# Kernel optimization log

Hardware: AMD Instinct MI355X
Metric: run time of the kernel (lower is better)

The kernel has to match this reference:

```python
import jax, jax.numpy as jnp
import numpy as np
import math

D_MODEL = 1024
NUM_HEADS = 16
D_HEAD = D_MODEL // NUM_HEADS


def setup_inputs() -> dict:
    key = jax.random.key(0)
    ks = jax.random.split(key, 15)
    B, S, D = 2, 2048, D_MODEL
    s = 1.0 / math.sqrt(D)
    inp = {
        'query': jax.random.normal(ks[0], (B, S, D), jnp.float32),
        'key': jax.random.normal(ks[1], (B, S, D), jnp.float32),
        'value': jax.random.normal(ks[2], (B, S, D), jnp.float32),
        'pos_embedding': jax.random.normal(ks[3], (B, S, D), jnp.float32),
        'Wq': jax.random.normal(ks[4], (D, D), jnp.float32) * s,
        'bq': jnp.zeros((D,), jnp.float32),
        'Wk': jax.random.normal(ks[5], (D, D), jnp.float32) * s,
        'bk': jnp.zeros((D,), jnp.float32),
        'Wv': jax.random.normal(ks[6], (D, D), jnp.float32) * s,
        'bv': jnp.zeros((D,), jnp.float32),
        'Wp': jax.random.normal(ks[7], (D, D), jnp.float32) * s,
        'bp': jnp.zeros((D,), jnp.float32),
        'Wo': jax.random.normal(ks[8], (D, D), jnp.float32) * s,
        'bo': jnp.zeros((D,), jnp.float32),
    }
    return inp


def _relative_shift(pos_score):
    # pos_score: [B, H, S1, S2] -> Transformer-XL pad/reshape/slice shift
    B, H, S1, S2 = pos_score.shape
    padded = jnp.pad(pos_score, ((0, 0), (0, 0), (0, 0), (1, 0)))  # [B,H,S1,S2+1]
    padded = padded.reshape(B, H, S2 + 1, S1)
    return padded[:, :, 1:].reshape(B, H, S1, S2)


def reference(query, key, value, pos_embedding, Wq, bq, Wk, bk, Wv, bv, Wp, bp, Wo, bo):
    B, S, D = query.shape
    H, Dh = NUM_HEADS, D_HEAD
    sqrt_dim = math.sqrt(D)

    q = (query @ Wq.T + bq).reshape(B, S, H, Dh)          # [B,S,H,Dh]
    k = (key @ Wk.T + bk).reshape(B, S, H, Dh)            # [B,S,H,Dh]
    v = (value @ Wv.T + bv).reshape(B, S, H, Dh)          # [B,S,H,Dh]
    p = (pos_embedding @ Wp.T + bp).reshape(B, S, H, Dh)  # [B,S,H,Dh]

    content_score = jnp.einsum('bqhd,bkhd->bhqk', q, k)   # [B,H,S,S]
    pos_score = jnp.einsum('bqhd,bkhd->bhqk', q, p)       # [B,H,S,S]
    pos_score = _relative_shift(pos_score)

    score = (content_score + pos_score) / sqrt_dim
    attn = jax.nn.softmax(score, axis=-1)
    context = jnp.einsum('bhqk,bkhd->bqhd', attn, v).reshape(B, S, D)
    return context @ Wo.T + bo
```

## Files before the change

### kernel.cpp

```cpp
#include <hip/hip_runtime.h>
#include <hip/hip_bf16.h>

#define S_LEN  2048
#define DMODEL 1024
#define NHEADS 16
#define DHEAD  64
#define TOKENS 4096
#define QSCALE 0.04508422f

typedef __attribute__((ext_vector_type(8))) short bf16x8;
typedef __attribute__((ext_vector_type(4))) float f32x4;

template <int M> struct IC { static constexpr int value = M; };

__device__ __forceinline__ float bf2f(unsigned short b) {
    union { unsigned u; float f; } v; v.u = ((unsigned)b) << 16;
    return v.f;
}
__device__ __forceinline__ unsigned cvt_pk_bf16(float lo, float hi) {
    unsigned r;
    asm("v_cvt_pk_bf16_f32 %0, %1, %2" : "=v"(r) : "v"(lo), "v"(hi));
    return r;
}
__device__ __forceinline__ unsigned short f2bf1(float x) {
    return (unsigned short)cvt_pk_bf16(x, x);
}
__device__ __forceinline__ void lds_fence() {
    asm volatile("s_waitcnt lgkmcnt(0)" ::: "memory");
    __builtin_amdgcn_sched_barrier(0);
}
__device__ __forceinline__ void gload_lds16(const void* g, void* l) {
    __builtin_amdgcn_global_load_lds(
        (const __attribute__((address_space(1))) void*)g,
        (__attribute__((address_space(3))) void*)l, 16, 0, 0);
}

__global__ __launch_bounds__(256) void proj_gemm(
    const float* __restrict__ x0, const float* __restrict__ x1,
    const float* __restrict__ x2, const float* __restrict__ x3,
    const float* __restrict__ w0, const float* __restrict__ w1,
    const float* __restrict__ w2, const float* __restrict__ w3,
    const float* __restrict__ b0, const float* __restrict__ b1,
    const float* __restrict__ b2, const float* __restrict__ b3,
    unsigned short* __restrict__ o0, unsigned short* __restrict__ o1,
    unsigned short* __restrict__ o2, unsigned short* __restrict__ o3)
{
    const int z = blockIdx.z;
    const float* X  = (z == 0) ? x0 : (z == 1) ? x1 : (z == 2) ? x2 : x3;
    const float* W  = (z == 0) ? w0 : (z == 1) ? w1 : (z == 2) ? w2 : w3;
    const float* Bv = (z == 0) ? b0 : (z == 1) ? b1 : (z == 2) ? b2 : b3;
    unsigned short* O = (z == 0) ? o0 : (z == 1) ? o1 : (z == 2) ? o2 : o3;

    __shared__ __align__(16) unsigned short At[128 * 40];
    __shared__ __align__(16) unsigned short Bt[128 * 40];

    const int tid  = threadIdx.x;
    const int lane = tid & 63;
    const int w    = tid >> 6;
    const int wr   = w & 1, wc = w >> 1;
    const int m0   = blockIdx.x * 128;
    const int n0   = blockIdx.y * 128;
    const int l16  = lane & 15, lq = lane >> 4;

    f32x4 acc[4][4];
    #pragma unroll
    for (int i = 0; i < 4; i++)
        #pragma unroll
        for (int j = 0; j < 4; j++) acc[i][j] = (f32x4){0.f, 0.f, 0.f, 0.f};

    for (int k0 = 0; k0 < DMODEL; k0 += 32) {
        __syncthreads();
        #pragma unroll
        for (int i = 0; i < 4; i++) {
            int e = tid + i * 256;
            int row = e >> 3, cg = e & 7;
            float4 va = *(const float4*)&X[(long)(m0 + row) * DMODEL + k0 + cg * 4];
            uint2 ua; ua.x = cvt_pk_bf16(va.x, va.y); ua.y = cvt_pk_bf16(va.z, va.w);
            *(uint2*)&At[row * 40 + cg * 4] = ua;
            float4 vb = *(const float4*)&W[(long)(n0 + row) * DMODEL + k0 + cg * 4];
            uint2 ub; ub.x = cvt_pk_bf16(vb.x, vb.y); ub.y = cvt_pk_bf16(vb.z, vb.w);
            *(uint2*)&Bt[row * 40 + cg * 4] = ub;
        }
        __syncthreads();
        bf16x8 af[4], bfr[4];
        #pragma unroll
        for (int f = 0; f < 4; f++) {
            af[f]  = *(const bf16x8*)&At[(64 * wr + 16 * f + l16) * 40 + 8 * lq];
            bfr[f] = *(const bf16x8*)&Bt[(64 * wc + 16 * f + l16) * 40 + 8 * lq];
        }
        #pragma unroll
        for (int i = 0; i < 4; i++)
            #pragma unroll
            for (int j = 0; j < 4; j++)
                acc[i][j] = __builtin_amdgcn_mfma_f32_16x16x32_bf16(af[i], bfr[j], acc[i][j], 0, 0, 0);
    }

    #pragma unroll
    for (int j = 0; j < 4; j++) {
        int n_g = n0 + 64 * wc + 16 * j + l16;
        float bias = Bv[n_g];
        int h = n_g >> 6, dh = n_g & 63;
        if (z == 2) {
            #pragma unroll
            for (int i = 0; i < 4; i++) {
                int m_g = m0 + 64 * wr + 16 * i + 4 * lq;
                int b = m_g >> 11, s = m_g & (S_LEN - 1);
                uint2 u;
                u.x = cvt_pk_bf16(acc[i][j][0] + bias, acc[i][j][1] + bias);
                u.y = cvt_pk_bf16(acc[i][j][2] + bias, acc[i][j][3] + bias);
                *(uint2*)&O[(long)(((b * NHEADS + h) * DHEAD) + dh) * S_LEN + s] = u;
            }
        } else {
            float scale = (z == 0) ? QSCALE : 1.0f;
            #pragma unroll
            for (int i = 0; i < 4; i++) {
                #pragma unroll
                for (int r = 0; r < 4; r++) {
                    int m_g = m0 + 64 * wr + 16 * i + 4 * lq + r;
                    int b = m_g >> 11, s = m_g & (S_LEN - 1);
                    O[(long)(((b * NHEADS + h) * S_LEN) + s) * DHEAD + dh] =
                        f2bf1((acc[i][j][r] + bias) * scale);
                }
            }
        }
    }
}

__global__ __launch_bounds__(512, 4) void rel_attn(
    const unsigned short* __restrict__ Q,
    const unsigned short* __restrict__ K,
    const unsigned short* __restrict__ VT,
    const unsigned short* __restrict__ P,
    unsigned short* __restrict__ CTX)
{
    __shared__ __align__(16) unsigned short Kb[64 * 64];
    __shared__ __align__(16) unsigned short P2b[256 * 64];
    __shared__ __align__(16) unsigned short WPb[8 * 1344];

    const int tid  = threadIdx.x;
    const int lane = tid & 63;
    const int w    = tid >> 6;
    const int l16  = lane & 15;
    const int lq   = lane >> 4;

    const int wg = ((blockIdx.x & 7) << 6) | (blockIdx.x >> 3);
    const int qt = wg & 15;
    const int bh = wg >> 4;
    const int q0 = qt << 7;
    const long baseQK = (long)bh * (S_LEN * DHEAD);
    const int gq_rel = 16 * w + l16;

    const unsigned short* Kbh = K + baseQK;
    const unsigned short* Pbh = P + baseQK;
    const unsigned short* Vl  = VT + baseQK + (long)l16 * S_LEN + 8 * lq;

    const int gx0 = ((0 + lq) ^ (l16 & 7)) * 8;
    const int gx1 = ((4 + lq) ^ (l16 & 7)) * 8;

    bf16x8 qf0[2], qf1[2];
    {
        const unsigned short* qrow = Q + baseQK + (long)(q0 + gq_rel) * DHEAD + 8 * lq;
        qf0[0] = *(const bf16x8*)(qrow);
        qf0[1] = *(const bf16x8*)(qrow + 32);
        qf1[0] = *(const bf16x8*)(qrow + DHEAD);
        qf1[1] = *(const bf16x8*)(qrow + DHEAD + 32);
    }

    const int srow = lane >> 3;
    const int sgr  = (lane & 7) ^ srow;
    auto stage_K = [&](int kr0) __attribute__((always_inline)) {
        const unsigned short* src = Kbh + (long)(kr0 + w * 8 + srow) * 64 + sgr * 8;
        gload_lds16(src, &Kb[(w * 8) * 64]);
    };
    auto stage_P2 = [&](int mfirst) __attribute__((always_inline)) {
        int m = mfirst + w * 8 + srow;
        int pr = m - ((m >= 2049) ? 2049 : 0);
        const unsigned short* src = Pbh + (long)pr * 64 + sgr * 8;
        gload_lds16(src, &P2b[(((mfirst & 255)) + w * 8) * 64]);
    };

    float mrow = -1e30f, lrow = 0.f;
    f32x4 oacc[4];
    #pragma unroll
    for (int f = 0; f < 4; f++) oacc[f] = (f32x4){0.f, 0.f, 0.f, 0.f};

    unsigned short* tw        = &WPb[w * 1344 + l16 * 84 + 4 * lq];
    const unsigned short* tr  = &WPb[w * 1344 + l16 * 83 + 15 + 4 * lq];
    unsigned short* pw        = &WPb[w * 1344 + l16 * 72 + 4 * lq];
    const unsigned short* prd = &WPb[w * 1344 + l16 * 72 + 8 * lq];

    const int W0 = 1920 - q0;
    stage_K(0);
    stage_P2(W0); stage_P2(W0 + 64); stage_P2(W0 + 128);
    __syncthreads();

    auto finish = [&](float (&sc)[4][4], bf16x8 (&vf)[2][4]) __attribute__((always_inline)) {
        float tmax = sc[0][0];
        #pragma unroll
        for (int fc = 0; fc < 4; ++fc)
            #pragma unroll
            for (int r = 0; r < 4; ++r) tmax = fmaxf(tmax, sc[fc][r]);
        tmax = fmaxf(tmax, __shfl_xor(tmax, 16, 64));
        tmax = fmaxf(tmax, __shfl_xor(tmax, 32, 64));
        float nm = fmaxf(mrow, tmax);
        float alpha = __builtin_amdgcn_exp2f(mrow - nm);
        mrow = nm;
        float pv[4][4];
        float rs = 0.f;
        #pragma unroll
        for (int fc = 0; fc < 4; ++fc)
            #pragma unroll
            for (int r = 0; r < 4; ++r) {
                float p = __builtin_amdgcn_exp2f(sc[fc][r] - nm);
                pv[fc][r] = p;
                rs += p;
            }
        rs += __shfl_xor(rs, 16, 64);
        rs += __shfl_xor(rs, 32, 64);
        lrow = lrow * alpha + rs;
        #pragma unroll
        for (int f = 0; f < 4; f++)
            #pragma unroll
            for (int r = 0; r < 4; r++) oacc[f][r] *= alpha;

        lds_fence();
        #pragma unroll
        for (int fc = 0; fc < 4; ++fc) {
            uint2 u;
            u.x = cvt_pk_bf16(pv[fc][0], pv[fc][1]);
            u.y = cvt_pk_bf16(pv[fc][2], pv[fc][3]);
            *(uint2*)(pw + 16 * fc) = u;
        }
        lds_fence();
        bf16x8 pfr[2];
        pfr[0] = *(const bf16x8*)(prd);
        pfr[1] = *(const bf16x8*)(prd + 32);

        #pragma unroll
        for (int kk = 0; kk < 2; ++kk)
            #pragma unroll
            for (int fa = 0; fa < 4; ++fa)
                oacc[fa] = __builtin_amdgcn_mfma_f32_16x16x32_bf16(vf[kk][fa], pfr[kk], oacc[fa], 0, 0, 0);
    };

    auto tile_pure = [&](auto mc, int ct, bool dz) __attribute__((always_inline)) {
        constexpr int MODE = decltype(mc)::value;
        const int c0 = ct << 6;
        const int mb = c0 - q0 + 2032 - 16 * w + l16;

        f32x4 cacc[4];
        #pragma unroll
        for (int f = 0; f < 4; f++) cacc[f] = (f32x4){0.f, 0.f, 0.f, 0.f};
        #pragma unroll
        for (int fc = 0; fc < 4; ++fc) {
            bf16x8 k0v = *(const bf16x8*)&Kb[(16 * fc + l16) * 64 + gx0];
            bf16x8 k1v = *(const bf16x8*)&Kb[(16 * fc + l16) * 64 + gx1];
            cacc[fc] = __builtin_amdgcn_mfma_f32_16x16x32_bf16(k0v, qf0[0], cacc[fc], 0, 0, 0);
            cacc[fc] = __builtin_amdgcn_mfma_f32_16x16x32_bf16(k1v, qf0[1], cacc[fc], 0, 0, 0);
        }

        f32x4 tacc[5];
        #pragma unroll
        for (int g = 0; g < 5; g++) tacc[g] = (f32x4){0.f, 0.f, 0.f, 0.f};
        #pragma unroll
        for (int cg = 0; cg < 5; ++cg) {
            int sb = ((mb + 16 * cg) & 255) * 64;
            bf16x8 p0 = *(const bf16x8*)&P2b[sb + gx0];
            bf16x8 p1 = *(const bf16x8*)&P2b[sb + gx1];
            tacc[cg] = __builtin_amdgcn_mfma_f32_16x16x32_bf16(
                p0, (MODE == 1) ? qf1[0] : qf0[0], tacc[cg], 0, 0, 0);
            tacc[cg] = __builtin_amdgcn_mfma_f32_16x16x32_bf16(
                p1, (MODE == 1) ? qf1[1] : qf0[1], tacc[cg], 0, 0, 0);
        }

        __syncthreads();
        if (ct < 31) { stage_K(c0 + 64); stage_P2(W0 + 192 + 64 * ct); }

        bf16x8 vf[2][4];
        #pragma unroll
        for (int kk = 0; kk < 2; ++kk)
            #pragma unroll
            for (int fa = 0; fa < 4; ++fa)
                vf[kk][fa] = *(const bf16x8*)(Vl + c0 + fa * (16 * S_LEN) + kk * 32);

        lds_fence();
        #pragma unroll
        for (int cg = 0; cg < 5; ++cg) {
            uint2 u;
            u.x = cvt_pk_bf16(tacc[cg][0], tacc[cg][1]);
            u.y = cvt_pk_bf16(tacc[cg][2], tacc[cg][3]);
            *(uint2*)(tw + 16 * cg) = u;
        }
        lds_fence();

        float sc[4][4];
        #pragma unroll
        for (int fc = 0; fc < 4; ++fc)
            #pragma unroll
            for (int r = 0; r < 4; ++r)
                sc[fc][r] = cacc[fc][r] + bf2f(tr[16 * fc + r]);
        if (MODE == 1 && dz && w == 7 && l16 == 15 && lq == 0)
            sc[0][0] = cacc[0][0];

        finish(sc, vf);
        __syncthreads();
    };

    auto tile_dual = [&](int ct) __attribute__((always_inline)) {
        const int c0 = ct << 6;
        const int mb = c0 - q0 + 2032 - 16 * w + l16;
        const int rel = q0 + gq_rel - c0;

        f32x4 cacc[4];
        #pragma unroll
        for (int f = 0; f < 4; f++) cacc[f] = (f32x4){0.f, 0.f, 0.f, 0.f};
        #pragma unroll
        for (int fc = 0; fc < 4; ++fc) {
            bf16x8 k0v = *(const bf16x8*)&Kb[(16 * fc + l16) * 64 + gx0];
            bf16x8 k1v = *(const bf16x8*)&Kb[(16 * fc + l16) * 64 + gx1];
            cacc[fc] = __builtin_amdgcn_mfma_f32_16x16x32_bf16(k0v, qf0[0], cacc[fc], 0, 0, 0);
            cacc[fc] = __builtin_amdgcn_mfma_f32_16x16x32_bf16(k1v, qf0[1], cacc[fc], 0, 0, 0);
        }

        f32x4 tacc[5];
        #pragma unroll
        for (int g = 0; g < 5; g++) tacc[g] = (f32x4){0.f, 0.f, 0.f, 0.f};
        #pragma unroll
        for (int cg = 0; cg < 5; ++cg) {
            int sb = ((mb + 16 * cg) & 255) * 64;
            bf16x8 p0 = *(const bf16x8*)&P2b[sb + gx0];
            bf16x8 p1 = *(const bf16x8*)&P2b[sb + gx1];
            tacc[cg] = __builtin_amdgcn_mfma_f32_16x16x32_bf16(p0, qf0[0], tacc[cg], 0, 0, 0);
            tacc[cg] = __builtin_amdgcn_mfma_f32_16x16x32_bf16(p1, qf0[1], tacc[cg], 0, 0, 0);
        }
        lds_fence();
        #pragma unroll
        for (int cg = 0; cg < 5; ++cg) {
            uint2 u;
            u.x = cvt_pk_bf16(tacc[cg][0], tacc[cg][1]);
            u.y = cvt_pk_bf16(tacc[cg][2], tacc[cg][3]);
            *(uint2*)(tw + 16 * cg) = u;
        }
        lds_fence();
        float v0[4][4];
        #pragma unroll
        for (int fc = 0; fc < 4; ++fc)
            #pragma unroll
            for (int r = 0; r < 4; ++r) v0[fc][r] = bf2f(tr[16 * fc + r]);
        lds_fence();

        f32x4 tb2[5];
        #pragma unroll
        for (int g = 0; g < 5; g++) tb2[g] = (f32x4){0.f, 0.f, 0.f, 0.f};
        #pragma unroll
        for (int cg = 0; cg < 5; ++cg) {
            int sb = ((mb + 16 * cg) & 255) * 64;
            bf16x8 p0 = *(const bf16x8*)&P2b[sb + gx0];
            bf16x8 p1 = *(const bf16x8*)&P2b[sb + gx1];
            tb2[cg] = __builtin_amdgcn_mfma_f32_16x16x32_bf16(p0, qf1[0], tb2[cg], 0, 0, 0);
            tb2[cg] = __builtin_amdgcn_mfma_f32_16x16x32_bf16(p1, qf1[1], tb2[cg], 0, 0, 0);
        }

        __syncthreads();
        if (ct < 31) { stage_K(c0 + 64); stage_P2(W0 + 192 + 64 * ct); }

        #pragma unroll
        for (int cg = 0; cg < 5; ++cg) {
            uint2 u;
            u.x = cvt_pk_bf16(tb2[cg][0], tb2[cg][1]);
            u.y = cvt_pk_bf16(tb2[cg][2], tb2[cg][3]);
            *(uint2*)(tw + 16 * cg) = u;
        }
        lds_fence();

        float sc[4][4];
        #pragma unroll
        for (int fc = 0; fc < 4; ++fc)
            #pragma unroll
            for (int r = 0; r < 4; ++r) {
                float vB = bf2f(tr[16 * fc + r]);
                int ci = 16 * fc + 4 * lq + r;
                float term = (ci == rel + 1) ? 0.f
                           : ((ci > rel) ? vB : v0[fc][r]);
                sc[fc][r] = cacc[fc][r] + term;
            }

        bf16x8 vf[2][4];
        #pragma unroll
        for (int kk = 0; kk < 2; ++kk)
            #pragma unroll
            for (int fa = 0; fa < 4; ++fa)
                vf[kk][fa] = *(const bf16x8*)(Vl + c0 + fa * (16 * S_LEN) + kk * 32);

        finish(sc, vf);
        __syncthreads();
    };

    const int dct = 2 * qt;
    for (int ct = 0; ct < dct; ++ct) tile_pure(IC<0>{}, ct, false);
    tile_dual(dct);
    tile_dual(dct + 1);
    for (int ct = dct + 2; ct < S_LEN / 64; ++ct)
        tile_pure(IC<1>{}, ct, ct == dct + 2);

    const int b = bh >> 4, h = bh & 15;
    const float rinv = 1.0f / lrow;
    unsigned short* op = CTX + ((long)(b * S_LEN + q0 + gq_rel) * NHEADS + h) * DHEAD + 4 * lq;
    #pragma unroll
    for (int fa = 0; fa < 4; ++fa) {
        uint2 u;
        u.x = cvt_pk_bf16(oacc[fa][0] * rinv, oacc[fa][1] * rinv);
        u.y = cvt_pk_bf16(oacc[fa][2] * rinv, oacc[fa][3] * rinv);
        *(uint2*)(op + 16 * fa) = u;
    }
}

__global__ __launch_bounds__(256) void out_gemm(
    const unsigned short* __restrict__ A,
    const float* __restrict__ W,
    const float* __restrict__ Bv,
    float* __restrict__ O)
{
    __shared__ __align__(16) unsigned short At[128 * 40];
    __shared__ __align__(16) unsigned short Bt[128 * 40];

    const int tid  = threadIdx.x;
    const int lane = tid & 63;
    const int w    = tid >> 6;
    const int wr   = w & 1, wc = w >> 1;
    const int m0   = blockIdx.x * 128;
    const int n0   = blockIdx.y * 128;
    const int l16  = lane & 15, lq = lane >> 4;

    f32x4 acc[4][4];
    #pragma unroll
    for (int i = 0; i < 4; i++)
        #pragma unroll
        for (int j = 0; j < 4; j++) acc[i][j] = (f32x4){0.f, 0.f, 0.f, 0.f};

    for (int k0 = 0; k0 < DMODEL; k0 += 32) {
        __syncthreads();
        #pragma unroll
        for (int i = 0; i < 2; i++) {
            int e = tid + i * 256;
            int row = e >> 2, sg = e & 3;
            *(float4*)&At[row * 40 + sg * 8] =
                *(const float4*)&A[(long)(m0 + row) * DMODEL + k0 + sg * 8];
        }
        #pragma unroll
        for (int i = 0; i < 4; i++) {
            int e = tid + i * 256;
            int row = e >> 3, cg = e & 7;
            float4 vb = *(const float4*)&W[(long)(n0 + row) * DMODEL + k0 + cg * 4];
            uint2 ub; ub.x = cvt_pk_bf16(vb.x, vb.y); ub.y = cvt_pk_bf16(vb.z, vb.w);
            *(uint2*)&Bt[row * 40 + cg * 4] = ub;
        }
        __syncthreads();
        bf16x8 af[4], bfr[4];
        #pragma unroll
        for (int f = 0; f < 4; f++) {
            af[f]  = *(const bf16x8*)&At[(64 * wr + 16 * f + l16) * 40 + 8 * lq];
            bfr[f] = *(const bf16x8*)&Bt[(64 * wc + 16 * f + l16) * 40 + 8 * lq];
        }
        #pragma unroll
        for (int i = 0; i < 4; i++)
            #pragma unroll
            for (int j = 0; j < 4; j++)
                acc[i][j] = __builtin_amdgcn_mfma_f32_16x16x32_bf16(af[i], bfr[j], acc[i][j], 0, 0, 0);
    }

    #pragma unroll
    for (int j = 0; j < 4; j++) {
        int n_g = n0 + 64 * wc + 16 * j + l16;
        float bias = Bv[n_g];
        #pragma unroll
        for (int i = 0; i < 4; i++) {
            #pragma unroll
            for (int r = 0; r < 4; r++) {
                int m_g = m0 + 64 * wr + 16 * i + 4 * lq + r;
                O[(long)m_g * DMODEL + n_g] = acc[i][j][r] + bias;
            }
        }
    }
}

extern "C" void kernel_launch(void* const* d_in, const int* in_sizes, int n_in,
                              void* d_out, int out_size, void* d_ws, size_t ws_size,
                              hipStream_t stream) {
    (void)in_sizes; (void)n_in; (void)out_size; (void)ws_size;
    const float* query = (const float*)d_in[0];
    const float* key_  = (const float*)d_in[1];
    const float* value = (const float*)d_in[2];
    const float* pos   = (const float*)d_in[3];
    const float* Wq = (const float*)d_in[4];  const float* bq = (const float*)d_in[5];
    const float* Wk = (const float*)d_in[6];  const float* bk = (const float*)d_in[7];
    const float* Wv = (const float*)d_in[8];  const float* bv = (const float*)d_in[9];
    const float* Wp = (const float*)d_in[10]; const float* bp = (const float*)d_in[11];
    const float* Wo = (const float*)d_in[12]; const float* bo = (const float*)d_in[13];
    float* out = (float*)d_out;

    const long NE = (long)TOKENS * DMODEL;
    unsigned short* qb = (unsigned short*)d_ws;
    unsigned short* kb = qb + NE;
    unsigned short* vb = kb + NE;
    unsigned short* pb = vb + NE;
    unsigned short* cx = pb + NE;

    proj_gemm<<<dim3(32, 8, 4), 256, 0, stream>>>(
        query, key_, value, pos, Wq, Wk, Wv, Wp, bq, bk, bv, bp, qb, kb, vb, pb);
    rel_attn<<<512, 512, 0, stream>>>(qb, kb, vb, pb, cx);
    out_gemm<<<dim3(32, 8), 256, 0, stream>>>(cx, Wo, bo, out);
}
```

Baseline: 272.1 us.

## Double-buffer K tiles and shrink attention blocks to 64 query rows

The relative-attention kernel now processes 64 query rows per block with 4 waves (1024 blocks of 256 threads) instead of 128 rows with 8 waves. K tiles are double-buffered in LDS, and the next tile's K/P loads plus the V register loads are issued at the start of each tile. This removes the mid-tile barrier and overlaps global-to-LDS staging with the MFMA work. In exchange, each block loads K/P for fewer query rows so there is less reuse, and the shared P ring buffer is now refilled without a barrier between reads and writes.

Result: slower. 356.0 us (+30.9%).

```diff
diff --git a/kernel.cpp b/kernel.cpp
--- a/kernel.cpp
+++ b/kernel.cpp
@@ -126,16 +126,16 @@
     }
 }
 
-__global__ __launch_bounds__(512, 4) void rel_attn(
+__global__ __launch_bounds__(256, 3) void rel_attn(
     const unsigned short* __restrict__ Q,
     const unsigned short* __restrict__ K,
     const unsigned short* __restrict__ VT,
     const unsigned short* __restrict__ P,
     unsigned short* __restrict__ CTX)
 {
-    __shared__ __align__(16) unsigned short Kb[64 * 64];
+    __shared__ __align__(16) unsigned short Kb[2 * 64 * 64];
     __shared__ __align__(16) unsigned short P2b[256 * 64];
-    __shared__ __align__(16) unsigned short WPb[8 * 1344];
+    __shared__ __align__(16) unsigned short WPb[4 * 1344];
 
     const int tid  = threadIdx.x;
     const int lane = tid & 63;
@@ -143,12 +143,12 @@
     const int l16  = lane & 15;
     const int lq   = lane >> 4;
 
-    const int wg = ((blockIdx.x & 7) << 6) | (blockIdx.x >> 3);
-    const int qt = wg & 15;
-    const int bh = wg >> 4;
-    const int q0 = qt << 7;
+    const int wg = ((blockIdx.x & 7) << 7) + (blockIdx.x >> 3);
+    const int qt = wg & 31;
+    const int bh = wg >> 5;
+    const int q0 = qt << 6;
     const long baseQK = (long)bh * (S_LEN * DHEAD);
-    const int gq_rel = 16 * w + l16;
+    const int qi_l = 16 * w + l16;
 
     const unsigned short* Kbh = K + baseQK;
     const unsigned short* Pbh = P + baseQK;
@@ -159,7 +159,7 @@
 
     bf16x8 qf0[2], qf1[2];
     {
-        const unsigned short* qrow = Q + baseQK + (long)(q0 + gq_rel) * DHEAD + 8 * lq;
+        const unsigned short* qrow = Q + baseQK + (long)(q0 + qi_l) * DHEAD + 8 * lq;
         qf0[0] = *(const bf16x8*)(qrow);
         qf0[1] = *(const bf16x8*)(qrow + 32);
         qf1[0] = *(const bf16x8*)(qrow + DHEAD);
@@ -168,15 +168,23 @@
 
     const int srow = lane >> 3;
     const int sgr  = (lane & 7) ^ srow;
-    auto stage_K = [&](int kr0) __attribute__((always_inline)) {
-        const unsigned short* src = Kbh + (long)(kr0 + w * 8 + srow) * 64 + sgr * 8;
-        gload_lds16(src, &Kb[(w * 8) * 64]);
+    auto stage_K = [&](int kr0, int buf) __attribute__((always_inline)) {
+        #pragma unroll
+        for (int j = 0; j < 2; ++j) {
+            int idx = w * 2 + j;
+            const unsigned short* src = Kbh + (long)(kr0 + idx * 8 + srow) * 64 + sgr * 8;
+            gload_lds16(src, &Kb[buf * 4096 + idx * 512]);
+        }
     };
     auto stage_P2 = [&](int mfirst) __attribute__((always_inline)) {
-        int m = mfirst + w * 8 + srow;
-        int pr = m - ((m >= 2049) ? 2049 : 0);
-        const unsigned short* src = Pbh + (long)pr * 64 + sgr * 8;
-        gload_lds16(src, &P2b[(((mfirst & 255)) + w * 8) * 64]);
+        #pragma unroll
+        for (int j = 0; j < 2; ++j) {
+            int idx = w * 2 + j;
+            int m = mfirst + idx * 8 + srow;
+            int pr = m - ((m >= 2049) ? 2049 : 0);
+            const unsigned short* src = Pbh + (long)pr * 64 + sgr * 8;
+            gload_lds16(src, &P2b[((mfirst + idx * 8) & 255) * 64]);
+        }
     };
 
     float mrow = -1e30f, lrow = 0.f;
@@ -189,9 +197,9 @@
     unsigned short* pw        = &WPb[w * 1344 + l16 * 72 + 4 * lq];
     const unsigned short* prd = &WPb[w * 1344 + l16 * 72 + 8 * lq];
 
-    const int W0 = 1920 - q0;
-    stage_K(0);
-    stage_P2(W0); stage_P2(W0 + 64); stage_P2(W0 + 128);
+    const int W0 = 1984 - q0;
+    stage_K(0, 0);
+    stage_P2(W0); stage_P2(W0 + 64);
     __syncthreads();
 
     auto finish = [&](float (&sc)[4][4], bf16x8 (&vf)[2][4]) __attribute__((always_inline)) {
@@ -246,15 +254,25 @@
     auto tile_pure = [&](auto mc, int ct, bool dz) __attribute__((always_inline)) {
         constexpr int MODE = decltype(mc)::value;
         const int c0 = ct << 6;
+        const int kb_ = (ct & 1) * 4096;
         const int mb = c0 - q0 + 2032 - 16 * w + l16;
 
+        bf16x8 vf[2][4];
+        #pragma unroll
+        for (int kk = 0; kk < 2; ++kk)
+            #pragma unroll
+            for (int fa = 0; fa < 4; ++fa)
+                vf[kk][fa] = *(const bf16x8*)(Vl + c0 + fa * (16 * S_LEN) + kk * 32);
+
+        if (ct < 31) { stage_K(c0 + 64, (ct & 1) ^ 1); stage_P2(W0 + 128 + 64 * ct); }
+
         f32x4 cacc[4];
         #pragma unroll
         for (int f = 0; f < 4; f++) cacc[f] = (f32x4){0.f, 0.f, 0.f, 0.f};
         #pragma unroll
         for (int fc = 0; fc < 4; ++fc) {
-            bf16x8 k0v = *(const bf16x8*)&Kb[(16 * fc + l16) * 64 + gx0];
-            bf16x8 k1v = *(const bf16x8*)&Kb[(16 * fc + l16) * 64 + gx1];
+            bf16x8 k0v = *(const bf16x8*)&Kb[kb_ + (16 * fc + l16) * 64 + gx0];
+            bf16x8 k1v = *(const bf16x8*)&Kb[kb_ + (16 * fc + l16) * 64 + gx1];
             cacc[fc] = __builtin_amdgcn_mfma_f32_16x16x32_bf16(k0v, qf0[0], cacc[fc], 0, 0, 0);
             cacc[fc] = __builtin_amdgcn_mfma_f32_16x16x32_bf16(k1v, qf0[1], cacc[fc], 0, 0, 0);
         }
@@ -273,16 +291,6 @@
                 p1, (MODE == 1) ? qf1[1] : qf0[1], tacc[cg], 0, 0, 0);
         }
 
-        __syncthreads();
-        if (ct < 31) { stage_K(c0 + 64); stage_P2(W0 + 192 + 64 * ct); }
-
-        bf16x8 vf[2][4];
-        #pragma unroll
-        for (int kk = 0; kk < 2; ++kk)
-            #pragma unroll
-            for (int fa = 0; fa < 4; ++fa)
-                vf[kk][fa] = *(const bf16x8*)(Vl + c0 + fa * (16 * S_LEN) + kk * 32);
-
         lds_fence();
         #pragma unroll
         for (int cg = 0; cg < 5; ++cg) {
@@ -299,7 +307,7 @@
             #pragma unroll
             for (int r = 0; r < 4; ++r)
                 sc[fc][r] = cacc[fc][r] + bf2f(tr[16 * fc + r]);
-        if (MODE == 1 && dz && w == 7 && l16 == 15 && lq == 0)
+        if (MODE == 1 && dz && qi_l == 63 && lq == 0)
             sc[0][0] = cacc[0][0];
 
         finish(sc, vf);
@@ -308,16 +316,18 @@
 
     auto tile_dual = [&](int ct) __attribute__((always_inline)) {
         const int c0 = ct << 6;
+        const int kb_ = (ct & 1) * 4096;
         const int mb = c0 - q0 + 2032 - 16 * w + l16;
-        const int rel = q0 + gq_rel - c0;
+
+        if (ct < 31) { stage_K(c0 + 64, (ct & 1) ^ 1); stage_P2(W0 + 128 + 64 * ct); }
 
         f32x4 cacc[4];
         #pragma unroll
         for (int f = 0; f < 4; f++) cacc[f] = (f32x4){0.f, 0.f, 0.f, 0.f};
         #pragma unroll
         for (int fc = 0; fc < 4; ++fc) {
-            bf16x8 k0v = *(const bf16x8*)&Kb[(16 * fc + l16) * 64 + gx0];
-            bf16x8 k1v = *(const bf16x8*)&Kb[(16 * fc + l16) * 64 + gx1];
+            bf16x8 k0v = *(const bf16x8*)&Kb[kb_ + (16 * fc + l16) * 64 + gx0];
+            bf16x8 k1v = *(const bf16x8*)&Kb[kb_ + (16 * fc + l16) * 64 + gx1];
             cacc[fc] = __builtin_amdgcn_mfma_f32_16x16x32_bf16(k0v, qf0[0], cacc[fc], 0, 0, 0);
             cacc[fc] = __builtin_amdgcn_mfma_f32_16x16x32_bf16(k1v, qf0[1], cacc[fc], 0, 0, 0);
         }
@@ -360,10 +370,6 @@
             tb2[cg] = __builtin_amdgcn_mfma_f32_16x16x32_bf16(p0, qf1[0], tb2[cg], 0, 0, 0);
             tb2[cg] = __builtin_amdgcn_mfma_f32_16x16x32_bf16(p1, qf1[1], tb2[cg], 0, 0, 0);
         }
-
-        __syncthreads();
-        if (ct < 31) { stage_K(c0 + 64); stage_P2(W0 + 192 + 64 * ct); }
-
         #pragma unroll
         for (int cg = 0; cg < 5; ++cg) {
             uint2 u;
@@ -378,10 +384,10 @@
         for (int fc = 0; fc < 4; ++fc)
             #pragma unroll
             for (int r = 0; r < 4; ++r) {
-                float vB = bf2f(tr[16 * fc + r]);
+                float v1 = bf2f(tr[16 * fc + r]);
                 int ci = 16 * fc + 4 * lq + r;
-                float term = (ci == rel + 1) ? 0.f
-                           : ((ci > rel) ? vB : v0[fc][r]);
+                float term = (ci == qi_l + 1) ? 0.f
+                           : ((ci > qi_l) ? v1 : v0[fc][r]);
                 sc[fc][r] = cacc[fc][r] + term;
             }
 
@@ -396,16 +402,16 @@
         __syncthreads();
     };
 
-    const int dct = 2 * qt;
-    for (int ct = 0; ct < dct; ++ct) tile_pure(IC<0>{}, ct, false);
-    tile_dual(dct);
-    tile_dual(dct + 1);
-    for (int ct = dct + 2; ct < S_LEN / 64; ++ct)
-        tile_pure(IC<1>{}, ct, ct == dct + 2);
+    for (int ct = 0; ct < qt; ++ct) tile_pure(IC<0>{}, ct, false);
+    tile_dual(qt);
+    if (qt < 31) {
+        tile_pure(IC<1>{}, qt + 1, true);
+        for (int ct = qt + 2; ct < S_LEN / 64; ++ct) tile_pure(IC<1>{}, ct, false);
+    }
 
     const int b = bh >> 4, h = bh & 15;
     const float rinv = 1.0f / lrow;
-    unsigned short* op = CTX + ((long)(b * S_LEN + q0 + gq_rel) * NHEADS + h) * DHEAD + 4 * lq;
+    unsigned short* op = CTX + ((long)(b * S_LEN + q0 + qi_l) * NHEADS + h) * DHEAD + 4 * lq;
     #pragma unroll
     for (int fa = 0; fa < 4; ++fa) {
         uint2 u;
@@ -508,6 +514,6 @@
 
     proj_gemm<<<dim3(32, 8, 4), 256, 0, stream>>>(
         query, key_, value, pos, Wq, Wk, Wv, Wp, bq, bk, bv, bp, qb, kb, vb, pb);
-    rel_attn<<<512, 512, 0, stream>>>(qb, kb, vb, pb, cx);
+    rel_attn<<<1024, 256, 0, stream>>>(qb, kb, vb, pb, cx);
     out_gemm<<<dim3(32, 8), 256, 0, stream>>>(cx, Wo, bo, out);
 }
```
